# Optimization experiments

Measured on AMD Instinct MI355X. Metric: run time of the kernel, lower is better.

Reference implementation:

```python
import jax, jax.numpy as jnp
import numpy as np

FILTER_K = 100  # filter_K from __init__
NUM_CLASSES = 1000


def setup_inputs() -> dict:
    key = jax.random.key(0)
    ks = jax.random.split(key, 7)
    B, Din, D, C, N = 256, 2048, 512, NUM_CLASSES, 50000
    x = jax.random.normal(ks[0], (B, Din), jnp.float32)
    Wf = jax.random.normal(ks[1], (Din, D), jnp.float32) * 0.02
    Wc = jax.random.normal(ks[2], (C, D), jnp.float32) * 0.05
    bc = jax.random.normal(ks[3], (C,), jnp.float32) * 0.01
    supports_in = jax.random.normal(ks[4], (N, D), jnp.float32)
    ent_in = jax.random.uniform(ks[5], (N,), jnp.float32)
    labels_idx = jax.random.randint(ks[6], (N,), 0, C)
    return {"x": x, "Wf": Wf, "Wc": Wc, "bc": bc,
            "supports_in": supports_in, "ent_in": ent_in, "labels_idx": labels_idx}


def _softmax_entropy(logits):
    # -(softmax * log_softmax).sum(1), computed stably in one pass
    logp = jax.nn.log_softmax(logits, axis=1)
    return -(jnp.exp(logp) * logp).sum(axis=1)


def reference(x, Wf, Wc, bc, supports_in, ent_in, labels_idx):
    C = Wc.shape[0]
    z = x @ Wf                    # featurizer: [B, D]
    p = z @ Wc.T + bc             # classifier logits: [B, C]
    yhat = jax.nn.one_hot(jnp.argmax(p, axis=1), C, dtype=z.dtype)
    ent_new = _softmax_entropy(p)
    labels_in = jax.nn.one_hot(labels_idx, C, dtype=z.dtype)

    # grow support memory
    supports = jnp.concatenate([supports_in, z], axis=0)   # [M, D]
    labels = jnp.concatenate([labels_in, yhat], axis=0)    # [M, C]
    ent = jnp.concatenate([ent_in, ent_new], axis=0)       # [M]

    # select_supports: per-class keep FILTER_K lowest-entropy entries.
    # Torch gathers a variable-size subset; equivalent fixed-shape form is a
    # boolean mask (non-selected rows contribute zero to the weights matmul).
    y = jnp.argmax(labels, axis=1)
    M = ent.shape[0]
    order = jnp.lexsort((ent, y))            # sort by class, then entropy
    y_sorted = y[order]
    # rank of each entry within its class segment
    rank = jnp.arange(M) - jnp.searchsorted(y_sorted, y_sorted, side='left')
    mask = jnp.zeros((M,), bool).at[order].set(rank < FILTER_K)
    maskf = mask.astype(z.dtype)

    # normalize supports row-wise (F.normalize, eps=1e-12), then masked matmul
    s_norm = supports / jnp.maximum(
        jnp.linalg.norm(supports, axis=1, keepdims=True), 1e-12)
    weights = (s_norm * maskf[:, None]).T @ (labels * maskf[:, None])  # [D, C]
    weights = weights / jnp.maximum(
        jnp.linalg.norm(weights, axis=0, keepdims=True), 1e-12)
    return z @ weights            # [B, C]
```

## Files before the change

### kernel.cpp

```cpp
#include <hip/hip_runtime.h>
#include <math.h>

#define BB   256
#define DIN  2048
#define DD   512
#define CC   1000
#define NN   50000
#define FILTER_K 100
#define SLOT 512
#define CSTRIDE 16

#define SK1  32
#define SKP  8
#define NBLK 512
#define NGRP 8
#define GSZ  (NBLK / NGRP)

#define Z_OFF     0
#define CNT_OFF   (Z_OFF + BB*DD)
#define EI_OFF    (CNT_OFF + 1024*CSTRIDE)
#define WN_OFF    (EI_OFF + CC*SLOT*2)
#define ZP_OFF    (WN_OFF + CC*DD)
#define PP_OFF    (ZP_OFF + SK1*BB*DD)

#define BAR_GRP(g)  ((1000 + 2*(g)) * CSTRIDE)
#define BAR_GLB     (1016 * CSTRIDE)
#define BAR_FLG     (1020 * CSTRIDE)

#define SMEM_F 3712

typedef float f32x4 __attribute__((ext_vector_type(4)));
typedef float f32x2 __attribute__((ext_vector_type(2)));

__device__ __forceinline__ void st_wc4(float* p, float4 v) {
  f32x4 w = {v.x, v.y, v.z, v.w};
  asm volatile("global_store_dwordx4 %0, %1, off sc0 sc1" :: "v"(p), "v"(w) : "memory");
}
__device__ __forceinline__ void st_wc2(float* p, float a, float b) {
  f32x2 w = {a, b};
  asm volatile("global_store_dwordx2 %0, %1, off sc0 sc1" :: "v"(p), "v"(w) : "memory");
}
__device__ __forceinline__ void st_wc1(float* p, float a) {
  asm volatile("global_store_dword %0, %1, off sc0 sc1" :: "v"(p), "v"(a) : "memory");
}
__device__ __forceinline__ float2 ld_cv2(const float2* p) {
  unsigned long long r = __hip_atomic_load((const unsigned long long*)p,
      __ATOMIC_RELAXED, __HIP_MEMORY_SCOPE_AGENT);
  float2 o;
  o.x = __uint_as_float((unsigned)(r & 0xffffffffULL));
  o.y = __uint_as_float((unsigned)(r >> 32));
  return o;
}
__device__ __forceinline__ int ld_ci(const int* p) {
  return __hip_atomic_load(p, __ATOMIC_RELAXED, __HIP_MEMORY_SCOPE_AGENT);
}

__device__ __forceinline__ void gsync(int* cnt, int epoch, int grp) {
  asm volatile("s_waitcnt vmcnt(0) lgkmcnt(0)" ::: "memory");
  __syncthreads();
  if (threadIdx.x == 0) {
    int t = __hip_atomic_fetch_add(&cnt[BAR_GRP(grp)], 1, __ATOMIC_RELAXED,
                                   __HIP_MEMORY_SCOPE_AGENT);
    bool set_flag = false;
    if (t == epoch * GSZ - 1) {
      int u = __hip_atomic_fetch_add(&cnt[BAR_GLB], 1, __ATOMIC_RELAXED,
                                     __HIP_MEMORY_SCOPE_AGENT);
      if (u == epoch * NGRP - 1) {
        __hip_atomic_store(&cnt[BAR_FLG], epoch, __ATOMIC_RELAXED,
                           __HIP_MEMORY_SCOPE_AGENT);
        set_flag = true;
      }
    }
    if (!set_flag) {
      while (__hip_atomic_load(&cnt[BAR_FLG], __ATOMIC_RELAXED,
                               __HIP_MEMORY_SCOPE_AGENT) < epoch)
        __builtin_amdgcn_s_sleep(2);
    }
  }
  __syncthreads();
}

__device__ __forceinline__ void do_class(
    int c, int tid, float* smem, const float* supports_in, const float* z,
    const float2* ei, const int* cnt, float* wn) {
  int*   sel = (int*)smem;
  float* se  = smem + SLOT;
  int*   si  = (int*)(smem + 2*SLOT);
  float (*part)[DD] = (float(*)[DD])(smem + 3*SLOT);
  float* tot = smem + 3*SLOT + 4*DD;
  const int lane = tid & 63, wid = tid >> 6;
  int n = ld_ci(&cnt[c * CSTRIDE]); if (n > SLOT) n = SLOT;

  int seln;
  if (n <= FILTER_K) {
    seln = n;
    for (int i = tid; i < n; i += 256)
      sel[i] = __float_as_int(ld_cv2(&ei[(size_t)c * SLOT + i]).y);
  } else {
    for (int i = tid; i < SLOT; i += 256) {
      if (i < n) {
        float2 pr = ld_cv2(&ei[(size_t)c * SLOT + i]);
        se[i] = pr.x; si[i] = __float_as_int(pr.y);
      } else { se[i] = INFINITY; si[i] = 0x7fffffff; }
    }
    __syncthreads();
    for (int k = 2; k <= SLOT; k <<= 1)
      for (int j = k >> 1; j > 0; j >>= 1) {
        for (int i = tid; i < SLOT; i += 256) {
          int ixj = i ^ j;
          if (ixj > i) {
            bool up = ((i & k) == 0);
            float e1 = se[i], e2 = se[ixj];
            int i1 = si[i], i2 = si[ixj];
            bool gt = (e1 > e2) || (e1 == e2 && i1 > i2);
            if (gt == up) { se[i] = e2; se[ixj] = e1; si[i] = i2; si[ixj] = i1; }
          }
        }
        __syncthreads();
      }
    seln = FILTER_K;
    for (int i = tid; i < FILTER_K; i += 256) sel[i] = si[i];
  }
  __syncthreads();
  const int seln_pad = (seln + 15) & ~15;
  if (seln > 0)
    for (int i = seln + tid; i < seln_pad; i += 256) sel[i] = sel[0];
  __syncthreads();

  float4 a0 = make_float4(0.f, 0.f, 0.f, 0.f), a1 = a0;
  for (int t = wid * 4; t < seln_pad; t += 16) {
    float4 u0[4], u1[4]; float s[4];
#pragma unroll
    for (int j = 0; j < 4; ++j) {
      int r = sel[t + j];
      const float4* p4 = (const float4*)((r < NN)
          ? supports_in + (size_t)r * DD : z + (size_t)(r - NN) * DD);
      u0[j] = p4[lane * 2]; u1[j] = p4[lane * 2 + 1];
    }
#pragma unroll
    for (int j = 0; j < 4; ++j)
      s[j] = u0[j].x * u0[j].x + u0[j].y * u0[j].y + u0[j].z * u0[j].z
           + u0[j].w * u0[j].w + u1[j].x * u1[j].x + u1[j].y * u1[j].y
           + u1[j].z * u1[j].z + u1[j].w * u1[j].w;
#pragma unroll
    for (int o = 1; o < 64; o <<= 1) {
#pragma unroll
      for (int j = 0; j < 4; ++j) s[j] += __shfl_xor(s[j], o, 64);
    }
#pragma unroll
    for (int j = 0; j < 4; ++j) {
      float sc = (t + j < seln) ? 1.0f / fmaxf(sqrtf(s[j]), 1e-12f) : 0.f;
      a0.x += u0[j].x * sc; a0.y += u0[j].y * sc;
      a0.z += u0[j].z * sc; a0.w += u0[j].w * sc;
      a1.x += u1[j].x * sc; a1.y += u1[j].y * sc;
      a1.z += u1[j].z * sc; a1.w += u1[j].w * sc;
    }
  }

  *(float4*)&part[wid][lane * 8] = a0;
  *(float4*)&part[wid][lane * 8 + 4] = a1;
  __syncthreads();
  const int d = tid * 2;
  float wx = part[0][d] + part[1][d] + part[2][d] + part[3][d];
  float wy = part[0][d + 1] + part[1][d + 1] + part[2][d + 1] + part[3][d + 1];
  float ss = wx * wx + wy * wy;
#pragma unroll
  for (int o = 1; o < 64; o <<= 1) ss += __shfl_xor(ss, o, 64);
  if (lane == 0) tot[wid] = ss;
  __syncthreads();
  float S = tot[0] + tot[1] + tot[2] + tot[3];
  float sc = 1.0f / fmaxf(sqrtf(S), 1e-12f);
  st_wc2(wn + (size_t)c * DD + 2 * tid, wx * sc, wy * sc);
}

__global__ __launch_bounds__(256, 2) void mega(
    const float* x, const float* Wf, const float* Wc, const float* bc,
    const float* supports_in, const float* ent_in, const int* labels_idx,
    float* out, float* ws) {
  __shared__ __align__(16) float smem[SMEM_F];
  float*  z     = ws + Z_OFF;
  int*    cnt   = (int*)(ws + CNT_OFF);
  float2* ei    = (float2*)(ws + EI_OFF);
  float*  wn    = ws + WN_OFF;
  float*  zpart = ws + ZP_OFF;
  float*  ppart = ws + PP_OFF;
  const int bid = blockIdx.x, tid = threadIdx.x;
  const int grp = bid >> 6;

  {
    float (*As)[68]  = (float(*)[68])smem;
    float (*Bs)[132] = (float(*)[132])(smem + 16 * 68);
    const int m0 = ((bid >> 2) & 3) * 64;
    const int n0 = (bid & 3) * 128;
    const int k0 = (bid >> 4) * 64;
    const int ar = tid >> 2, ac = (tid & 3) * 4;
    const int br = tid >> 4, bcn = (tid & 15) * 8;
    const int tm = (tid >> 4) * 4, tn = (tid & 15) * 4;
    float acc[4][8] = {};
    float4 av  = *(const float4*)&x[(size_t)(m0 + ar) * DIN + k0 + ac];
    float4 bv0 = *(const float4*)&Wf[(size_t)(k0 + br) * DD + n0 + bcn];
    float4 bv1 = *(const float4*)&Wf[(size_t)(k0 + br) * DD + n0 + bcn + 4];
    for (int kk = 0; kk < 64; kk += 16) {
      __syncthreads();
      As[ac + 0][ar] = av.x; As[ac + 1][ar] = av.y;
      As[ac + 2][ar] = av.z; As[ac + 3][ar] = av.w;
      *(float4*)&Bs[br][bcn] = bv0;
      *(float4*)&Bs[br][bcn + 4] = bv1;
      __syncthreads();
      if (kk + 16 < 64) {
        av  = *(const float4*)&x[(size_t)(m0 + ar) * DIN + k0 + kk + 16 + ac];
        bv0 = *(const float4*)&Wf[(size_t)(k0 + kk + 16 + br) * DD + n0 + bcn];
        bv1 = *(const float4*)&Wf[(size_t)(k0 + kk + 16 + br) * DD + n0 + bcn + 4];
      }
#pragma unroll
      for (int q = 0; q < 16; ++q) {
        float4 a  = *(const float4*)&As[q][tm];
        float4 b0 = *(const float4*)&Bs[q][tn];
        float4 b1 = *(const float4*)&Bs[q][tn + 64];
        float aa[4] = {a.x, a.y, a.z, a.w};
        float bb[8] = {b0.x, b0.y, b0.z, b0.w, b1.x, b1.y, b1.z, b1.w};
#pragma unroll
        for (int i = 0; i < 4; ++i)
#pragma unroll
          for (int j = 0; j < 8; ++j) acc[i][j] += aa[i] * bb[j];
      }
    }
    float* Cb = zpart + (size_t)(bid >> 4) * BB * DD;
#pragma unroll
    for (int i = 0; i < 4; ++i) {
      st_wc4(&Cb[(size_t)(m0 + tm + i) * DD + n0 + tn],
             make_float4(acc[i][0], acc[i][1], acc[i][2], acc[i][3]));
      st_wc4(&Cb[(size_t)(m0 + tm + i) * DD + n0 + 64 + tn],
             make_float4(acc[i][4], acc[i][5], acc[i][6], acc[i][7]));
    }
  }
  gsync(cnt, 1, grp);

  if (bid < 128) {
    const int n4 = BB * DD / 4;
    int i = bid * 256 + tid;
    if (i < n4) {
      const float4* p4 = (const float4*)zpart;
      float4 a = p4[i];
#pragma unroll
      for (int s = 1; s < SK1; ++s) {
        float4 b = p4[(size_t)s * n4 + i];
        a.x += b.x; a.y += b.y; a.z += b.z; a.w += b.w;
      }
      st_wc4(z + 4 * (size_t)i, a);
    }
  } else if (bid < 324) {
    int m = (bid - 128) * 256 + tid;
    if (m < NN) {
      int c = labels_idx[m];
      int pos = atomicAdd(&cnt[c * CSTRIDE], 1);
      if (pos < SLOT) {
        st_wc2((float*)&ei[(size_t)c * SLOT + pos], ent_in[m], __int_as_float(m));
      }
    }
  }
  gsync(cnt, 2, grp);

  {
    float (*As)[68] = (float(*)[68])smem;
    float (*Bs)[68] = (float(*)[68])(smem + 16 * 68);
    const int n0 = (bid & 15) * 64;
    const int m0 = ((bid >> 4) & 3) * 64;
    const int ks = bid >> 6;
    const int k0 = ks * 64;
    const int ar = tid >> 2, ac = (tid & 3) * 4;
    const int tm = (tid >> 4) * 4, tn = (tid & 15) * 4;
    float acc[4][4] = {};
    float4 av = *(const float4*)&z[(size_t)(m0 + ar) * DD + k0 + ac];
    float4 bv = make_float4(0.f, 0.f, 0.f, 0.f);
    if (n0 + ar < CC) bv = *(const float4*)&Wc[(size_t)(n0 + ar) * DD + k0 + ac];
    for (int kk = 0; kk < 64; kk += 16) {
      __syncthreads();
      As[ac + 0][ar] = av.x; As[ac + 1][ar] = av.y;
      As[ac + 2][ar] = av.z; As[ac + 3][ar] = av.w;
      Bs[ac + 0][ar] = bv.x; Bs[ac + 1][ar] = bv.y;
      Bs[ac + 2][ar] = bv.z; Bs[ac + 3][ar] = bv.w;
      __syncthreads();
      if (kk + 16 < 64) {
        av = *(const float4*)&z[(size_t)(m0 + ar) * DD + k0 + kk + 16 + ac];
        if (n0 + ar < CC)
          bv = *(const float4*)&Wc[(size_t)(n0 + ar) * DD + k0 + kk + 16 + ac];
      }
#pragma unroll
      for (int q = 0; q < 16; ++q) {
        float4 a = *(const float4*)&As[q][tm];
        float4 b = *(const float4*)&Bs[q][tn];
        float aa[4] = {a.x, a.y, a.z, a.w};
        float bb[4] = {b.x, b.y, b.z, b.w};
#pragma unroll
        for (int i = 0; i < 4; ++i)
#pragma unroll
          for (int j = 0; j < 4; ++j) acc[i][j] += aa[i] * bb[j];
      }
    }
    float* Cb = ppart + (size_t)ks * BB * CC;
#pragma unroll
    for (int i = 0; i < 4; ++i) {
      int n = n0 + tn;
      if (n + 3 < CC) {
        st_wc4(&Cb[(size_t)(m0 + tm + i) * CC + n],
               make_float4(acc[i][0], acc[i][1], acc[i][2], acc[i][3]));
      } else {
#pragma unroll
        for (int j = 0; j < 4; ++j)
          if (n + j < CC) st_wc1(&Cb[(size_t)(m0 + tm + i) * CC + n + j], acc[i][j]);
      }
    }
  }
  gsync(cnt, 3, grp);

  if (bid < BB) {
    float* smv = smem; int* smi = (int*)(smem + 4);
    float* ssm = smem + 8; float* tsm = smem + 12;
    const int b = bid;
    const int lane = tid & 63, wid = tid >> 6;
    float r[4];
    float mv = -INFINITY; int mi = 0x7fffffff;
#pragma unroll
    for (int i = 0; i < 4; ++i) {
      int c = tid + 256 * i;
      if (c < CC) {
        float v = bc[c];
#pragma unroll
        for (int s = 0; s < SKP; ++s)
          v += ppart[(size_t)s * BB * CC + (size_t)b * CC + c];
        r[i] = v;
      } else r[i] = -INFINITY;
      if (r[i] > mv) { mv = r[i]; mi = c; }
    }
#pragma unroll
    for (int o = 32; o > 0; o >>= 1) {
      float ov = __shfl_down(mv, o, 64);
      int oi = __shfl_down(mi, o, 64);
      if (ov > mv || (ov == mv && oi < mi)) { mv = ov; mi = oi; }
    }
    if (lane == 0) { smv[wid] = mv; smi[wid] = mi; }
    __syncthreads();
    if (tid == 0) {
#pragma unroll
      for (int w = 1; w < 4; ++w)
        if (smv[w] > smv[0] || (smv[w] == smv[0] && smi[w] < smi[0])) {
          smv[0] = smv[w]; smi[0] = smi[w];
        }
    }
    __syncthreads();
    const float m = smv[0]; const int am = smi[0];
    float s = 0.f, t = 0.f;
#pragma unroll
    for (int i = 0; i < 4; ++i) {
      if (tid + 256 * i < CC) {
        float u = r[i] - m;
        float e = expf(u);
        s += e; t += u * e;
      }
    }
#pragma unroll
    for (int o = 32; o > 0; o >>= 1) {
      s += __shfl_down(s, o, 64);
      t += __shfl_down(t, o, 64);
    }
    if (lane == 0) { ssm[wid] = s; tsm[wid] = t; }
    __syncthreads();
    if (tid == 0) {
      float S = ssm[0] + ssm[1] + ssm[2] + ssm[3];
      float T = tsm[0] + tsm[1] + tsm[2] + tsm[3];
      float ent = logf(S) - T / S;
      int pos = atomicAdd(&cnt[am * CSTRIDE], 1);
      if (pos < SLOT) {
        st_wc2((float*)&ei[(size_t)am * SLOT + pos], ent, __int_as_float(NN + b));
      }
    }
  }
  gsync(cnt, 4, grp);

  do_class(bid, tid, smem, supports_in, z, ei, cnt, wn);
  __syncthreads();
  if (bid + 512 < CC)
    do_class(bid + 512, tid, smem, supports_in, z, ei, cnt, wn);
  gsync(cnt, 5, grp);

  if (bid < 256) {
    float (*As)[20] = (float(*)[20])smem;
    float (*Bs)[68] = (float(*)[68])(smem + 16 * 20);
    const int m0 = (bid >> 4) * 16;
    const int n0 = (bid & 15) * 64;
    const int arow = tid >> 4, ak = tid & 15;
    const int br = tid >> 2, bcl = (tid & 3) * 4;
    const int tr = tid >> 4, tn4 = (tid & 15) * 4;
    float acc[4] = {};
    float av = z[(size_t)(m0 + arow) * DD + ak];
    float4 bv = make_float4(0.f, 0.f, 0.f, 0.f);
    if (n0 + br < CC) bv = *(const float4*)&wn[(size_t)(n0 + br) * DD + bcl];
    for (int k0 = 0; k0 < DD; k0 += 16) {
      __syncthreads();
      As[ak][arow] = av;
      Bs[bcl + 0][br] = bv.x; Bs[bcl + 1][br] = bv.y;
      Bs[bcl + 2][br] = bv.z; Bs[bcl + 3][br] = bv.w;
      __syncthreads();
      if (k0 + 16 < DD) {
        av = z[(size_t)(m0 + arow) * DD + k0 + 16 + ak];
        if (n0 + br < CC)
          bv = *(const float4*)&wn[(size_t)(n0 + br) * DD + k0 + 16 + bcl];
      }
#pragma unroll
      for (int q = 0; q < 16; ++q) {
        float a = As[q][tr];
        float4 b = *(const float4*)&Bs[q][tn4];
        acc[0] += a * b.x; acc[1] += a * b.y;
        acc[2] += a * b.z; acc[3] += a * b.w;
      }
    }
    int n = n0 + tn4;
    if (n + 3 < CC) {
      *(float4*)&out[(size_t)(m0 + tr) * CC + n] =
          make_float4(acc[0], acc[1], acc[2], acc[3]);
    } else {
#pragma unroll
      for (int j = 0; j < 4; ++j)
        if (n + j < CC) out[(size_t)(m0 + tr) * CC + n + j] = acc[j];
    }
  }
}

extern "C" void kernel_launch(void* const* d_in, const int* in_sizes, int n_in,
                              void* d_out, int out_size, void* d_ws, size_t ws_size,
                              hipStream_t stream) {
  (void)in_sizes; (void)n_in; (void)out_size; (void)ws_size;
  const float* x           = (const float*)d_in[0];
  const float* Wf          = (const float*)d_in[1];
  const float* Wc          = (const float*)d_in[2];
  const float* bc          = (const float*)d_in[3];
  const float* supports_in = (const float*)d_in[4];
  const float* ent_in      = (const float*)d_in[5];
  const int*   labels_idx  = (const int*)d_in[6];
  float* out = (float*)d_out;
  float* W = (float*)d_ws;
  int* cnt = (int*)(W + CNT_OFF);

  hipMemsetAsync(cnt, 0, 1024 * CSTRIDE * sizeof(int), stream);
  hipLaunchKernelGGL(mega, dim3(NBLK), dim3(256), 0, stream,
                     x, Wf, Wc, bc, supports_in, ent_in, labels_idx, out, W);
}
```

Before: 218.9 us.

## Split final z·W GEMM across all blocks with split-K partials and reduction

The final output GEMM, previously computed by 256 blocks each looping over the full K=512, is now split-K across all 512 blocks (8 K-slices of 64) writing partials to a new workspace region, followed by an extra grid sync and a float4 reduction into the output. The class-aggregation loop now processes 8 support rows per wave instead of 4 for more memory-level parallelism, and the logits reduction is vectorised with float4 loads. This trades an additional global barrier and partial-buffer traffic for better occupancy of the last stage, and the wider unroll raises register pressure.

```diff
diff --git a/kernel.cpp b/kernel.cpp
--- a/kernel.cpp
+++ b/kernel.cpp
@@ -12,6 +12,7 @@
 
 #define SK1  32
 #define SKP  8
+#define SKO  8
 #define NBLK 512
 #define NGRP 8
 #define GSZ  (NBLK / NGRP)
@@ -22,6 +23,7 @@
 #define WN_OFF    (EI_OFF + CC*SLOT*2)
 #define ZP_OFF    (WN_OFF + CC*DD)
 #define PP_OFF    (ZP_OFF + SK1*BB*DD)
+#define OP_OFF    (PP_OFF + SKP*BB*CC)
 
 #define BAR_GRP(g)  ((1000 + 2*(g)) * CSTRIDE)
 #define BAR_GLB     (1016 * CSTRIDE)
@@ -122,33 +124,33 @@
     for (int i = tid; i < FILTER_K; i += 256) sel[i] = si[i];
   }
   __syncthreads();
-  const int seln_pad = (seln + 15) & ~15;
+  const int seln_pad = (seln + 31) & ~31;
   if (seln > 0)
     for (int i = seln + tid; i < seln_pad; i += 256) sel[i] = sel[0];
   __syncthreads();
 
   float4 a0 = make_float4(0.f, 0.f, 0.f, 0.f), a1 = a0;
-  for (int t = wid * 4; t < seln_pad; t += 16) {
-    float4 u0[4], u1[4]; float s[4];
-#pragma unroll
-    for (int j = 0; j < 4; ++j) {
+  for (int t = wid * 8; t < seln_pad; t += 32) {
+    float4 u0[8], u1[8]; float s[8];
+#pragma unroll
+    for (int j = 0; j < 8; ++j) {
       int r = sel[t + j];
       const float4* p4 = (const float4*)((r < NN)
           ? supports_in + (size_t)r * DD : z + (size_t)(r - NN) * DD);
       u0[j] = p4[lane * 2]; u1[j] = p4[lane * 2 + 1];
     }
 #pragma unroll
-    for (int j = 0; j < 4; ++j)
+    for (int j = 0; j < 8; ++j)
       s[j] = u0[j].x * u0[j].x + u0[j].y * u0[j].y + u0[j].z * u0[j].z
            + u0[j].w * u0[j].w + u1[j].x * u1[j].x + u1[j].y * u1[j].y
            + u1[j].z * u1[j].z + u1[j].w * u1[j].w;
 #pragma unroll
     for (int o = 1; o < 64; o <<= 1) {
 #pragma unroll
-      for (int j = 0; j < 4; ++j) s[j] += __shfl_xor(s[j], o, 64);
-    }
-#pragma unroll
-    for (int j = 0; j < 4; ++j) {
+      for (int j = 0; j < 8; ++j) s[j] += __shfl_xor(s[j], o, 64);
+    }
+#pragma unroll
+    for (int j = 0; j < 8; ++j) {
       float sc = (t + j < seln) ? 1.0f / fmaxf(sqrtf(s[j]), 1e-12f) : 0.f;
       a0.x += u0[j].x * sc; a0.y += u0[j].y * sc;
       a0.z += u0[j].z * sc; a0.w += u0[j].w * sc;
@@ -171,6 +173,55 @@
   float S = tot[0] + tot[1] + tot[2] + tot[3];
   float sc = 1.0f / fmaxf(sqrtf(S), 1e-12f);
   st_wc2(wn + (size_t)c * DD + 2 * tid, wx * sc, wy * sc);
+}
+
+__device__ __forceinline__ void gemm_abt_tile(
+    const float* __restrict__ A, const float* __restrict__ Bm,
+    float* __restrict__ Cb, float* smem, int tid, int m0, int n0, int k0) {
+  float (*As)[68] = (float(*)[68])smem;
+  float (*Bs)[68] = (float(*)[68])(smem + 16 * 68);
+  const int ar = tid >> 2, ac = (tid & 3) * 4;
+  const int tm = (tid >> 4) * 4, tn = (tid & 15) * 4;
+  float acc[4][4] = {};
+  float4 av = *(const float4*)&A[(size_t)(m0 + ar) * DD + k0 + ac];
+  float4 bv = make_float4(0.f, 0.f, 0.f, 0.f);
+  if (n0 + ar < CC) bv = *(const float4*)&Bm[(size_t)(n0 + ar) * DD + k0 + ac];
+  for (int kk = 0; kk < 64; kk += 16) {
+    __syncthreads();
+    As[ac + 0][ar] = av.x; As[ac + 1][ar] = av.y;
+    As[ac + 2][ar] = av.z; As[ac + 3][ar] = av.w;
+    Bs[ac + 0][ar] = bv.x; Bs[ac + 1][ar] = bv.y;
+    Bs[ac + 2][ar] = bv.z; Bs[ac + 3][ar] = bv.w;
+    __syncthreads();
+    if (kk + 16 < 64) {
+      av = *(const float4*)&A[(size_t)(m0 + ar) * DD + k0 + kk + 16 + ac];
+      if (n0 + ar < CC)
+        bv = *(const float4*)&Bm[(size_t)(n0 + ar) * DD + k0 + kk + 16 + ac];
+    }
+#pragma unroll
+    for (int q = 0; q < 16; ++q) {
+      float4 a = *(const float4*)&As[q][tm];
+      float4 b = *(const float4*)&Bs[q][tn];
+      float aa[4] = {a.x, a.y, a.z, a.w};
+      float bb[4] = {b.x, b.y, b.z, b.w};
+#pragma unroll
+      for (int i = 0; i < 4; ++i)
+#pragma unroll
+        for (int j = 0; j < 4; ++j) acc[i][j] += aa[i] * bb[j];
+    }
+  }
+#pragma unroll
+  for (int i = 0; i < 4; ++i) {
+    int n = n0 + tn;
+    if (n + 3 < CC) {
+      st_wc4(&Cb[(size_t)(m0 + tm + i) * CC + n],
+             make_float4(acc[i][0], acc[i][1], acc[i][2], acc[i][3]));
+    } else {
+#pragma unroll
+      for (int j = 0; j < 4; ++j)
+        if (n + j < CC) st_wc1(&Cb[(size_t)(m0 + tm + i) * CC + n + j], acc[i][j]);
+    }
+  }
 }
 
 __global__ __launch_bounds__(256, 2) void mega(
@@ -184,6 +235,7 @@
   float*  wn    = ws + WN_OFF;
   float*  zpart = ws + ZP_OFF;
   float*  ppart = ws + PP_OFF;
+  float*  opart = ws + OP_OFF;
   const int bid = blockIdx.x, tid = threadIdx.x;
   const int grp = bid >> 6;
 
@@ -262,55 +314,9 @@
   gsync(cnt, 2, grp);
 
   {
-    float (*As)[68] = (float(*)[68])smem;
-    float (*Bs)[68] = (float(*)[68])(smem + 16 * 68);
-    const int n0 = (bid & 15) * 64;
-    const int m0 = ((bid >> 4) & 3) * 64;
     const int ks = bid >> 6;
-    const int k0 = ks * 64;
-    const int ar = tid >> 2, ac = (tid & 3) * 4;
-    const int tm = (tid >> 4) * 4, tn = (tid & 15) * 4;
-    float acc[4][4] = {};
-    float4 av = *(const float4*)&z[(size_t)(m0 + ar) * DD + k0 + ac];
-    float4 bv = make_float4(0.f, 0.f, 0.f, 0.f);
-    if (n0 + ar < CC) bv = *(const float4*)&Wc[(size_t)(n0 + ar) * DD + k0 + ac];
-    for (int kk = 0; kk < 64; kk += 16) {
-      __syncthreads();
-      As[ac + 0][ar] = av.x; As[ac + 1][ar] = av.y;
-      As[ac + 2][ar] = av.z; As[ac + 3][ar] = av.w;
-      Bs[ac + 0][ar] = bv.x; Bs[ac + 1][ar] = bv.y;
-      Bs[ac + 2][ar] = bv.z; Bs[ac + 3][ar] = bv.w;
-      __syncthreads();
-      if (kk + 16 < 64) {
-        av = *(const float4*)&z[(size_t)(m0 + ar) * DD + k0 + kk + 16 + ac];
-        if (n0 + ar < CC)
-          bv = *(const float4*)&Wc[(size_t)(n0 + ar) * DD + k0 + kk + 16 + ac];
-      }
-#pragma unroll
-      for (int q = 0; q < 16; ++q) {
-        float4 a = *(const float4*)&As[q][tm];
-        float4 b = *(const float4*)&Bs[q][tn];
-        float aa[4] = {a.x, a.y, a.z, a.w};
-        float bb[4] = {b.x, b.y, b.z, b.w};
-#pragma unroll
-        for (int i = 0; i < 4; ++i)
-#pragma unroll
-          for (int j = 0; j < 4; ++j) acc[i][j] += aa[i] * bb[j];
-      }
-    }
-    float* Cb = ppart + (size_t)ks * BB * CC;
-#pragma unroll
-    for (int i = 0; i < 4; ++i) {
-      int n = n0 + tn;
-      if (n + 3 < CC) {
-        st_wc4(&Cb[(size_t)(m0 + tm + i) * CC + n],
-               make_float4(acc[i][0], acc[i][1], acc[i][2], acc[i][3]));
-      } else {
-#pragma unroll
-        for (int j = 0; j < 4; ++j)
-          if (n + j < CC) st_wc1(&Cb[(size_t)(m0 + tm + i) * CC + n + j], acc[i][j]);
-      }
-    }
+    gemm_abt_tile(z, Wc, ppart + (size_t)ks * BB * CC, smem, tid,
+                  ((bid >> 4) & 3) * 64, (bid & 15) * 64, ks * 64);
   }
   gsync(cnt, 3, grp);
 
@@ -319,20 +325,21 @@
     float* ssm = smem + 8; float* tsm = smem + 12;
     const int b = bid;
     const int lane = tid & 63, wid = tid >> 6;
-    float r[4];
+    const int cbase = tid * 4;
+    float rr[4];
     float mv = -INFINITY; int mi = 0x7fffffff;
-#pragma unroll
-    for (int i = 0; i < 4; ++i) {
-      int c = tid + 256 * i;
-      if (c < CC) {
-        float v = bc[c];
-#pragma unroll
-        for (int s = 0; s < SKP; ++s)
-          v += ppart[(size_t)s * BB * CC + (size_t)b * CC + c];
-        r[i] = v;
-      } else r[i] = -INFINITY;
-      if (r[i] > mv) { mv = r[i]; mi = c; }
-    }
+    if (cbase < CC) {
+      float4 v = *(const float4*)&bc[cbase];
+#pragma unroll
+      for (int s = 0; s < SKP; ++s) {
+        float4 pv = *(const float4*)&ppart[(size_t)s * BB * CC + (size_t)b * CC + cbase];
+        v.x += pv.x; v.y += pv.y; v.z += pv.z; v.w += pv.w;
+      }
+      rr[0] = v.x; rr[1] = v.y; rr[2] = v.z; rr[3] = v.w;
+#pragma unroll
+      for (int j = 0; j < 4; ++j)
+        if (rr[j] > mv) { mv = rr[j]; mi = cbase + j; }
+    } else { rr[0] = rr[1] = rr[2] = rr[3] = -INFINITY; }
 #pragma unroll
     for (int o = 32; o > 0; o >>= 1) {
       float ov = __shfl_down(mv, o, 64);
@@ -351,10 +358,10 @@
     __syncthreads();
     const float m = smv[0]; const int am = smi[0];
     float s = 0.f, t = 0.f;
-#pragma unroll
-    for (int i = 0; i < 4; ++i) {
-      if (tid + 256 * i < CC) {
-        float u = r[i] - m;
+    if (cbase < CC) {
+#pragma unroll
+      for (int j = 0; j < 4; ++j) {
+        float u = rr[j] - m;
         float e = expf(u);
         s += e; t += u * e;
       }
@@ -384,45 +391,23 @@
     do_class(bid + 512, tid, smem, supports_in, z, ei, cnt, wn);
   gsync(cnt, 5, grp);
 
+  {
+    const int ks = bid >> 6;
+    gemm_abt_tile(z, wn, opart + (size_t)ks * BB * CC, smem, tid,
+                  ((bid >> 4) & 3) * 64, (bid & 15) * 64, ks * 64);
+  }
+  gsync(cnt, 6, grp);
+
   if (bid < 256) {
-    float (*As)[20] = (float(*)[20])smem;
-    float (*Bs)[68] = (float(*)[68])(smem + 16 * 20);
-    const int m0 = (bid >> 4) * 16;
-    const int n0 = (bid & 15) * 64;
-    const int arow = tid >> 4, ak = tid & 15;
-    const int br = tid >> 2, bcl = (tid & 3) * 4;
-    const int tr = tid >> 4, tn4 = (tid & 15) * 4;
-    float acc[4] = {};
-    float av = z[(size_t)(m0 + arow) * DD + ak];
-    float4 bv = make_float4(0.f, 0.f, 0.f, 0.f);
-    if (n0 + br < CC) bv = *(const float4*)&wn[(size_t)(n0 + br) * DD + bcl];
-    for (int k0 = 0; k0 < DD; k0 += 16) {
-      __syncthreads();
-      As[ak][arow] = av;
-      Bs[bcl + 0][br] = bv.x; Bs[bcl + 1][br] = bv.y;
-      Bs[bcl + 2][br] = bv.z; Bs[bcl + 3][br] = bv.w;
-      __syncthreads();
-      if (k0 + 16 < DD) {
-        av = z[(size_t)(m0 + arow) * DD + k0 + 16 + ak];
-        if (n0 + br < CC)
-          bv = *(const float4*)&wn[(size_t)(n0 + br) * DD + k0 + 16 + bcl];
-      }
-#pragma unroll
-      for (int q = 0; q < 16; ++q) {
-        float a = As[q][tr];
-        float4 b = *(const float4*)&Bs[q][tn4];
-        acc[0] += a * b.x; acc[1] += a * b.y;
-        acc[2] += a * b.z; acc[3] += a * b.w;
-      }
-    }
-    int n = n0 + tn4;
-    if (n + 3 < CC) {
-      *(float4*)&out[(size_t)(m0 + tr) * CC + n] =
-          make_float4(acc[0], acc[1], acc[2], acc[3]);
-    } else {
-#pragma unroll
-      for (int j = 0; j < 4; ++j)
-        if (n + j < CC) out[(size_t)(m0 + tr) * CC + n + j] = acc[j];
+    const int cbase = tid * 4;
+    if (cbase < CC) {
+      float4 a = *(const float4*)&opart[(size_t)bid * CC + cbase];
+#pragma unroll
+      for (int s = 1; s < SKO; ++s) {
+        float4 b = *(const float4*)&opart[(size_t)s * BB * CC + (size_t)bid * CC + cbase];
+        a.x += b.x; a.y += b.y; a.z += b.z; a.w += b.w;
+      }
+      *(float4*)&out[(size_t)bid * CC + cbase] = a;
     }
   }
 }
```

New measurement: 218.7 us. About the same (-0.1%).

## Use hierarchical grid barrier with per-group flags and vectorize logits reduction

Applied to the files above, without the earlier changes.

Reworks the grid barrier so only one leader block per group polls the global flag, then releases its group through a per-group flag on a separate cache line. All other blocks spin on their group flag, which is meant to cut contention on a single global location. Counters are spread 1024 ints apart, which enlarges the memset. The logits reduction now reads float4 per thread over contiguous classes, and the classifier GEMM tile is moved into a helper function.

```diff
diff --git a/kernel.cpp b/kernel.cpp
--- a/kernel.cpp
+++ b/kernel.cpp
@@ -18,14 +18,16 @@
 
 #define Z_OFF     0
 #define CNT_OFF   (Z_OFF + BB*DD)
-#define EI_OFF    (CNT_OFF + 1024*CSTRIDE)
+#define BAR_BASE  16384
+#define ARR_IDX(g)   (BAR_BASE + (g)*1024)
+#define GFLG_IDX(g)  (BAR_BASE + (8+(g))*1024)
+#define GLBC_IDX     (BAR_BASE + 16*1024)
+#define GLBF_IDX     (BAR_BASE + 17*1024)
+#define CNT_INTS  (16384 + 20*1024)
+#define EI_OFF    (CNT_OFF + CNT_INTS)
 #define WN_OFF    (EI_OFF + CC*SLOT*2)
 #define ZP_OFF    (WN_OFF + CC*DD)
 #define PP_OFF    (ZP_OFF + SK1*BB*DD)
-
-#define BAR_GRP(g)  ((1000 + 2*(g)) * CSTRIDE)
-#define BAR_GLB     (1016 * CSTRIDE)
-#define BAR_FLG     (1020 * CSTRIDE)
 
 #define SMEM_F 3712
 
@@ -55,26 +57,29 @@
   return __hip_atomic_load(p, __ATOMIC_RELAXED, __HIP_MEMORY_SCOPE_AGENT);
 }
 
-__device__ __forceinline__ void gsync(int* cnt, int epoch, int grp) {
+__device__ __forceinline__ void gsync(int* cnt, int epoch, int grp, bool leader) {
   asm volatile("s_waitcnt vmcnt(0) lgkmcnt(0)" ::: "memory");
   __syncthreads();
   if (threadIdx.x == 0) {
-    int t = __hip_atomic_fetch_add(&cnt[BAR_GRP(grp)], 1, __ATOMIC_RELAXED,
+    int t = __hip_atomic_fetch_add(&cnt[ARR_IDX(grp)], 1, __ATOMIC_RELAXED,
                                    __HIP_MEMORY_SCOPE_AGENT);
-    bool set_flag = false;
     if (t == epoch * GSZ - 1) {
-      int u = __hip_atomic_fetch_add(&cnt[BAR_GLB], 1, __ATOMIC_RELAXED,
+      int u = __hip_atomic_fetch_add(&cnt[GLBC_IDX], 1, __ATOMIC_RELAXED,
                                      __HIP_MEMORY_SCOPE_AGENT);
-      if (u == epoch * NGRP - 1) {
-        __hip_atomic_store(&cnt[BAR_FLG], epoch, __ATOMIC_RELAXED,
+      if (u == epoch * NGRP - 1)
+        __hip_atomic_store(&cnt[GLBF_IDX], epoch, __ATOMIC_RELAXED,
                            __HIP_MEMORY_SCOPE_AGENT);
-        set_flag = true;
-      }
-    }
-    if (!set_flag) {
-      while (__hip_atomic_load(&cnt[BAR_FLG], __ATOMIC_RELAXED,
+    }
+    if (leader) {
+      while (__hip_atomic_load(&cnt[GLBF_IDX], __ATOMIC_RELAXED,
                                __HIP_MEMORY_SCOPE_AGENT) < epoch)
-        __builtin_amdgcn_s_sleep(2);
+        __builtin_amdgcn_s_sleep(4);
+      __hip_atomic_store(&cnt[GFLG_IDX(grp)], epoch, __ATOMIC_RELAXED,
+                         __HIP_MEMORY_SCOPE_AGENT);
+    } else {
+      while (__hip_atomic_load(&cnt[GFLG_IDX(grp)], __ATOMIC_RELAXED,
+                               __HIP_MEMORY_SCOPE_AGENT) < epoch)
+        __builtin_amdgcn_s_sleep(8);
     }
   }
   __syncthreads();
@@ -173,6 +178,55 @@
   st_wc2(wn + (size_t)c * DD + 2 * tid, wx * sc, wy * sc);
 }
 
+__device__ __forceinline__ void gemm_abt_tile(
+    const float* __restrict__ A, const float* __restrict__ Bm,
+    float* __restrict__ Cb, float* smem, int tid, int m0, int n0, int k0) {
+  float (*As)[68] = (float(*)[68])smem;
+  float (*Bs)[68] = (float(*)[68])(smem + 16 * 68);
+  const int ar = tid >> 2, ac = (tid & 3) * 4;
+  const int tm = (tid >> 4) * 4, tn = (tid & 15) * 4;
+  float acc[4][4] = {};
+  float4 av = *(const float4*)&A[(size_t)(m0 + ar) * DD + k0 + ac];
+  float4 bv = make_float4(0.f, 0.f, 0.f, 0.f);
+  if (n0 + ar < CC) bv = *(const float4*)&Bm[(size_t)(n0 + ar) * DD + k0 + ac];
+  for (int kk = 0; kk < 64; kk += 16) {
+    __syncthreads();
+    As[ac + 0][ar] = av.x; As[ac + 1][ar] = av.y;
+    As[ac + 2][ar] = av.z; As[ac + 3][ar] = av.w;
+    Bs[ac + 0][ar] = bv.x; Bs[ac + 1][ar] = bv.y;
+    Bs[ac + 2][ar] = bv.z; Bs[ac + 3][ar] = bv.w;
+    __syncthreads();
+    if (kk + 16 < 64) {
+      av = *(const float4*)&A[(size_t)(m0 + ar) * DD + k0 + kk + 16 + ac];
+      if (n0 + ar < CC)
+        bv = *(const float4*)&Bm[(size_t)(n0 + ar) * DD + k0 + kk + 16 + ac];
+    }
+#pragma unroll
+    for (int q = 0; q < 16; ++q) {
+      float4 a = *(const float4*)&As[q][tm];
+      float4 b = *(const float4*)&Bs[q][tn];
+      float aa[4] = {a.x, a.y, a.z, a.w};
+      float bb[4] = {b.x, b.y, b.z, b.w};
+#pragma unroll
+      for (int i = 0; i < 4; ++i)
+#pragma unroll
+        for (int j = 0; j < 4; ++j) acc[i][j] += aa[i] * bb[j];
+    }
+  }
+#pragma unroll
+  for (int i = 0; i < 4; ++i) {
+    int n = n0 + tn;
+    if (n + 3 < CC) {
+      st_wc4(&Cb[(size_t)(m0 + tm + i) * CC + n],
+             make_float4(acc[i][0], acc[i][1], acc[i][2], acc[i][3]));
+    } else {
+#pragma unroll
+      for (int j = 0; j < 4; ++j)
+        if (n + j < CC) st_wc1(&Cb[(size_t)(m0 + tm + i) * CC + n + j], acc[i][j]);
+    }
+  }
+}
+
 __global__ __launch_bounds__(256, 2) void mega(
     const float* x, const float* Wf, const float* Wc, const float* bc,
     const float* supports_in, const float* ent_in, const int* labels_idx,
@@ -186,6 +240,7 @@
   float*  ppart = ws + PP_OFF;
   const int bid = blockIdx.x, tid = threadIdx.x;
   const int grp = bid >> 6;
+  const bool leader = (bid & 63) == 0;
 
   {
     float (*As)[68]  = (float(*)[68])smem;
@@ -234,7 +289,7 @@
              make_float4(acc[i][4], acc[i][5], acc[i][6], acc[i][7]));
     }
   }
-  gsync(cnt, 1, grp);
+  gsync(cnt, 1, grp, leader);
 
   if (bid < 128) {
     const int n4 = BB * DD / 4;
@@ -259,80 +314,35 @@
       }
     }
   }
-  gsync(cnt, 2, grp);
+  gsync(cnt, 2, grp, leader);
 
   {
-    float (*As)[68] = (float(*)[68])smem;
-    float (*Bs)[68] = (float(*)[68])(smem + 16 * 68);
-    const int n0 = (bid & 15) * 64;
-    const int m0 = ((bid >> 4) & 3) * 64;
     const int ks = bid >> 6;
-    const int k0 = ks * 64;
-    const int ar = tid >> 2, ac = (tid & 3) * 4;
-    const int tm = (tid >> 4) * 4, tn = (tid & 15) * 4;
-    float acc[4][4] = {};
-    float4 av = *(const float4*)&z[(size_t)(m0 + ar) * DD + k0 + ac];
-    float4 bv = make_float4(0.f, 0.f, 0.f, 0.f);
-    if (n0 + ar < CC) bv = *(const float4*)&Wc[(size_t)(n0 + ar) * DD + k0 + ac];
-    for (int kk = 0; kk < 64; kk += 16) {
-      __syncthreads();
-      As[ac + 0][ar] = av.x; As[ac + 1][ar] = av.y;
-      As[ac + 2][ar] = av.z; As[ac + 3][ar] = av.w;
-      Bs[ac + 0][ar] = bv.x; Bs[ac + 1][ar] = bv.y;
-      Bs[ac + 2][ar] = bv.z; Bs[ac + 3][ar] = bv.w;
-      __syncthreads();
-      if (kk + 16 < 64) {
-        av = *(const float4*)&z[(size_t)(m0 + ar) * DD + k0 + kk + 16 + ac];
-        if (n0 + ar < CC)
-          bv = *(const float4*)&Wc[(size_t)(n0 + ar) * DD + k0 + kk + 16 + ac];
-      }
-#pragma unroll
-      for (int q = 0; q < 16; ++q) {
-        float4 a = *(const float4*)&As[q][tm];
-        float4 b = *(const float4*)&Bs[q][tn];
-        float aa[4] = {a.x, a.y, a.z, a.w};
-        float bb[4] = {b.x, b.y, b.z, b.w};
-#pragma unroll
-        for (int i = 0; i < 4; ++i)
-#pragma unroll
-          for (int j = 0; j < 4; ++j) acc[i][j] += aa[i] * bb[j];
-      }
-    }
-    float* Cb = ppart + (size_t)ks * BB * CC;
-#pragma unroll
-    for (int i = 0; i < 4; ++i) {
-      int n = n0 + tn;
-      if (n + 3 < CC) {
-        st_wc4(&Cb[(size_t)(m0 + tm + i) * CC + n],
-               make_float4(acc[i][0], acc[i][1], acc[i][2], acc[i][3]));
-      } else {
-#pragma unroll
-        for (int j = 0; j < 4; ++j)
-          if (n + j < CC) st_wc1(&Cb[(size_t)(m0 + tm + i) * CC + n + j], acc[i][j]);
-      }
-    }
-  }
-  gsync(cnt, 3, grp);
+    gemm_abt_tile(z, Wc, ppart + (size_t)ks * BB * CC, smem, tid,
+                  ((bid >> 4) & 3) * 64, (bid & 15) * 64, ks * 64);
+  }
+  gsync(cnt, 3, grp, leader);
 
   if (bid < BB) {
     float* smv = smem; int* smi = (int*)(smem + 4);
     float* ssm = smem + 8; float* tsm = smem + 12;
     const int b = bid;
     const int lane = tid & 63, wid = tid >> 6;
-    float r[4];
+    const int cbase = tid * 4;
+    float rr[4];
     float mv = -INFINITY; int mi = 0x7fffffff;
-#pragma unroll
-    for (int i = 0; i < 4; ++i) {
-      int c = tid + 256 * i;
-      if (c < CC) {
-        float v = bc[c];
-#pragma unroll
-        for (int s = 0; s < SKP; ++s)
-          v += ppart[(size_t)s * BB * CC + (size_t)b * CC + c];
-        r[i] = v;
-      } else r[i] = -INFINITY;
-      if (r[i] > mv) { mv = r[i]; mi = c; }
-    }
+    if (cbase < CC) {
+      float4 v = *(const float4*)&bc[cbase];
+#pragma unroll
+      for (int s = 0; s < SKP; ++s) {
+        float4 pv = *(const float4*)&ppart[(size_t)s * BB * CC + (size_t)b * CC + cbase];
+        v.x += pv.x; v.y += pv.y; v.z += pv.z; v.w += pv.w;
+      }
+      rr[0] = v.x; rr[1] = v.y; rr[2] = v.z; rr[3] = v.w;
+#pragma unroll
+      for (int j = 0; j < 4; ++j)
+        if (rr[j] > mv) { mv = rr[j]; mi = cbase + j; }
+    } else { rr[0] = rr[1] = rr[2] = rr[3] = -INFINITY; }
 #pragma unroll
     for (int o = 32; o > 0; o >>= 1) {
       float ov = __shfl_down(mv, o, 64);
@@ -351,10 +361,10 @@
     __syncthreads();
     const float m = smv[0]; const int am = smi[0];
     float s = 0.f, t = 0.f;
-#pragma unroll
-    for (int i = 0; i < 4; ++i) {
-      if (tid + 256 * i < CC) {
-        float u = r[i] - m;
+    if (cbase < CC) {
+#pragma unroll
+      for (int j = 0; j < 4; ++j) {
+        float u = rr[j] - m;
         float e = expf(u);
         s += e; t += u * e;
       }
@@ -376,13 +386,13 @@
       }
     }
   }
-  gsync(cnt, 4, grp);
+  gsync(cnt, 4, grp, leader);
 
   do_class(bid, tid, smem, supports_in, z, ei, cnt, wn);
   __syncthreads();
   if (bid + 512 < CC)
     do_class(bid + 512, tid, smem, supports_in, z, ei, cnt, wn);
-  gsync(cnt, 5, grp);
+  gsync(cnt, 5, grp, leader);
 
   if (bid < 256) {
     float (*As)[20] = (float(*)[20])smem;
@@ -442,7 +452,7 @@
   float* W = (float*)d_ws;
   int* cnt = (int*)(W + CNT_OFF);
 
-  hipMemsetAsync(cnt, 0, 1024 * CSTRIDE * sizeof(int), stream);
+  hipMemsetAsync(cnt, 0, CNT_INTS * sizeof(int), stream);
   hipLaunchKernelGGL(mega, dim3(NBLK), dim3(256), 0, stream,
                      x, Wf, Wc, bc, supports_in, ent_in, labels_idx, out, W);
 }
```

After: 222.3 us. Within noise of the previous version (+1.6%).
